# Kernel optimization log

Measured on AMD Instinct MI355X. Metric: run time of the kernel, lower is better.

Reference implementation:

```python
import jax, jax.numpy as jnp
import numpy as np
import math

E = 1024      # embed_dim
H = 16        # num_heads
HD = E // H   # head_dim
NBITS = 8


def fake_quant(x, n_bits=NBITS):
    """Symmetric per-tensor fake quantize with STE (clamp/round/dequant)."""
    qmax = 2.0 ** (n_bits - 1) - 1.0
    qmin = -(2.0 ** (n_bits - 1))
    scale = jnp.maximum(jnp.max(jnp.abs(x)) / qmax, 1e-8)
    xq = jnp.round(jnp.clip(x / scale, qmin, qmax)) * scale
    return x + jax.lax.stop_gradient(xq - x)


def setup_inputs() -> dict:
    key = jax.random.key(0)
    ks = jax.random.split(key, 7)
    L, B = 2048, 2
    query = jax.random.normal(ks[0], (L, B, E), dtype=jnp.float32)
    k_in = jax.random.normal(ks[1], (L, B, E), dtype=jnp.float32)
    v_in = jax.random.normal(ks[2], (L, B, E), dtype=jnp.float32)
    in_w = jax.random.normal(ks[3], (3 * E, E), dtype=jnp.float32) * (1.0 / math.sqrt(E))
    in_b = jax.random.normal(ks[4], (3 * E,), dtype=jnp.float32) * 0.01
    out_w = jax.random.normal(ks[5], (E, E), dtype=jnp.float32) * (1.0 / math.sqrt(E))
    out_b = jax.random.normal(ks[6], (E,), dtype=jnp.float32) * 0.01
    return {"query": query, "key": k_in, "value": v_in,
            "in_w": in_w, "in_b": in_b, "out_w": out_w, "out_b": out_b}


def reference(query, key, value, in_w, in_b, out_w, out_b):
    # NOTE: the original module ignores `key`/`value` (pure self-attention on query),
    # and its attn / softmax fake-quant lines are dead statements (results discarded).
    L, B, _ = query.shape
    Wi = fake_quant(in_w)
    Wo = fake_quant(out_w)
    # input projection: [L,B,3E]
    X = jnp.einsum('lbe,fe->lbf', query, Wi) + in_b
    X = fake_quant(X)
    Q, K, V = jnp.split(X, 3, axis=-1)  # each [L,B,E]
    # [L, B*H, HD] -> [B*H, L, HD]
    q = Q.reshape(L, B * H, HD).transpose(1, 0, 2)
    k = K.reshape(L, B * H, HD).transpose(1, 0, 2)
    v = V.reshape(L, B * H, HD).transpose(1, 0, 2)
    q = q / math.sqrt(HD)
    q = fake_quant(q)
    attn = jnp.einsum('bqd,bkd->bqk', q, k)          # [B*H, L, L]
    attn = jax.nn.softmax(attn, axis=-1)
    heads = jnp.einsum('bqk,bkd->bqd', attn, v)      # [B*H, L, HD]
    heads = fake_quant(heads)
    # [B*H, L, HD] -> [L, B*H, HD] -> [L*B, E]
    heads_r = heads.transpose(1, 0, 2).reshape(L * B, E)
    y = heads_r @ Wo.T + out_b
    y = y.reshape(L, B, E)
    return fake_quant(y)
```

## Files before the change

kernel.cpp:

```cpp
#include <hip/hip_runtime.h>
#include <math.h>

#define L_SEQ 2048
#define BATCH 2
#define EMB 1024
#define NH 16
#define HDIM 64
#define F3 3072
#define NROWS 4096

typedef __bf16 bf16_t;
typedef short s16x8 __attribute__((ext_vector_type(8)));
typedef float f32x4 __attribute__((ext_vector_type(4)));

#define MFMA16(a, b, c) __builtin_amdgcn_mfma_f32_16x16x32_bf16(a, b, c, 0, 0, 0)


__device__ __forceinline__ float u2f(unsigned u) { return __uint_as_float(u); }

__device__ __forceinline__ unsigned short bfb(bf16_t x) {
  union { bf16_t b; unsigned short u; } c; c.b = x; return c.u;
}

__device__ __forceinline__ void gload16(const bf16_t* g, bf16_t* lds) {
  __builtin_amdgcn_global_load_lds((const __attribute__((address_space(1))) void*)g,
                                   (__attribute__((address_space(3))) void*)lds, 16, 0, 0);
}

__device__ __forceinline__ void blockmax_commit(float m, unsigned* slot) {
  #pragma unroll
  for (int o = 1; o < 64; o <<= 1) m = fmaxf(m, __shfl_xor(m, o));
  __shared__ float sm_[4];
  if ((threadIdx.x & 63) == 0) sm_[threadIdx.x >> 6] = m;
  __syncthreads();
  if (threadIdx.x == 0) {
    float mm = fmaxf(fmaxf(sm_[0], sm_[1]), fmaxf(sm_[2], sm_[3]));
    atomicMax(slot, __float_as_uint(mm));
  }
}

__global__ __launch_bounds__(256) void absmax_k(const float* __restrict__ x, int n4,
                                                unsigned* __restrict__ slot) {
  const float4* x4 = (const float4*)x;
  float m = 0.0f;
  for (int i = blockIdx.x * blockDim.x + threadIdx.x; i < n4; i += gridDim.x * blockDim.x) {
    float4 v = x4[i];
    m = fmaxf(m, fmaxf(fmaxf(fabsf(v.x), fabsf(v.y)), fmaxf(fabsf(v.z), fabsf(v.w))));
  }
  blockmax_commit(m, slot);
}

__global__ __launch_bounds__(256) void quantf_k(const float* __restrict__ x,
                                                bf16_t* __restrict__ y, int n4,
                                                const unsigned* __restrict__ slots, int sloti) {
  float s = fmaxf(u2f(slots[sloti]) / 127.0f, 1e-8f);
  const float4* x4 = (const float4*)x;
  for (int i = blockIdx.x * blockDim.x + threadIdx.x; i < n4; i += gridDim.x * blockDim.x) {
    float4 v = x4[i];
    bf16_t o[4];
    o[0] = (bf16_t)rintf(fminf(fmaxf(v.x / s, -128.0f), 127.0f));
    o[1] = (bf16_t)rintf(fminf(fmaxf(v.y / s, -128.0f), 127.0f));
    o[2] = (bf16_t)rintf(fminf(fmaxf(v.z / s, -128.0f), 127.0f));
    o[3] = (bf16_t)rintf(fminf(fmaxf(v.w / s, -128.0f), 127.0f));
    *(uint2*)&y[(size_t)i * 4] = *(uint2*)o;
  }
}

__global__ __launch_bounds__(256) void quantX_k(const float* __restrict__ x,
                                                bf16_t* __restrict__ y,
                                                unsigned* __restrict__ slots) {
  float s = fmaxf(u2f(slots[2]) / 127.0f, 1e-8f);
  float qm = 0.0f;
  const int n8 = NROWS * F3 / 8;
  for (int i = blockIdx.x * blockDim.x + threadIdx.x; i < n8; i += gridDim.x * blockDim.x) {
    float4 v0 = *(const float4*)&x[(size_t)i * 8];
    float4 v1 = *(const float4*)&x[(size_t)i * 8 + 4];
    float vv[8] = {v0.x, v0.y, v0.z, v0.w, v1.x, v1.y, v1.z, v1.w};
    bf16_t o[8];
    float lm = 0.0f;
    #pragma unroll
    for (int j = 0; j < 8; ++j) {
      float q = rintf(fminf(fmaxf(vv[j] / s, -128.0f), 127.0f));
      o[j] = (bf16_t)q;
      lm = fmaxf(lm, fabsf(q));
    }
    if ((i % 384) < 128) qm = fmaxf(qm, lm);
    *(uint4*)&y[(size_t)i * 8] = *(uint4*)o;
  }
  blockmax_commit(qm, slots + 3);
}

__global__ __launch_bounds__(256) void quant_k(float* __restrict__ x, int n4,
                                               const unsigned* __restrict__ slots, int sloti) {
  float s = fmaxf(u2f(slots[sloti]) / 127.0f, 1e-8f);
  float4* x4 = (float4*)x;
  for (int i = blockIdx.x * blockDim.x + threadIdx.x; i < n4; i += gridDim.x * blockDim.x) {
    float4 v = x4[i];
    v.x = rintf(fminf(fmaxf(v.x / s, -128.0f), 127.0f)) * s;
    v.y = rintf(fminf(fmaxf(v.y / s, -128.0f), 127.0f)) * s;
    v.z = rintf(fminf(fmaxf(v.z / s, -128.0f), 127.0f)) * s;
    v.w = rintf(fminf(fmaxf(v.w / s, -128.0f), 127.0f)) * s;
    x4[i] = v;
  }
}

__global__ __launch_bounds__(256) void split_k(const float* __restrict__ x,
                                               bf16_t* __restrict__ hi,
                                               bf16_t* __restrict__ lo, int n4) {
  const float4* x4 = (const float4*)x;
  for (int i = blockIdx.x * blockDim.x + threadIdx.x; i < n4; i += gridDim.x * blockDim.x) {
    float4 v = x4[i];
    bf16_t h[4], l[4];
    float vv[4] = {v.x, v.y, v.z, v.w};
    #pragma unroll
    for (int j = 0; j < 4; ++j) {
      h[j] = (bf16_t)vv[j];
      l[j] = (bf16_t)(vv[j] - (float)h[j]);
    }
    *(uint2*)&hi[(size_t)i * 4] = *(uint2*)h;
    *(uint2*)&lo[(size_t)i * 4] = *(uint2*)l;
  }
}

__global__ __launch_bounds__(256) void vtrans_k(const bf16_t* __restrict__ X,
                                                bf16_t* __restrict__ Vt) {
  __shared__ __align__(16) bf16_t tile[64][72];
  int tt = blockIdx.x, bh = blockIdx.y;
  int b = bh >> 4, h = bh & 15;
  int t = threadIdx.x;
  #pragma unroll
  for (int i = 0; i < 2; ++i) {
    int s = t + i * 256;
    int tok = s >> 3, seg = s & 7;
    uint4 v = *(const uint4*)&X[((size_t)(tt * 64 + tok) * BATCH + b) * F3 + 2 * EMB + h * HDIM + seg * 8];
    int segs = seg ^ (tok >> 3);
    *(uint4*)&tile[tok][segs * 8] = v;
  }
  __syncthreads();
  #pragma unroll
  for (int i = 0; i < 2; ++i) {
    int s = t + i * 256;
    int d = s >> 3, tseg = s & 7;
    bf16_t o[8];
    #pragma unroll
    for (int e = 0; e < 8; ++e) {
      int tok = tseg * 8 + e;
      o[e] = tile[tok][(((d >> 3) ^ (tok >> 3)) << 3) | (d & 7)];
    }
    *(uint4*)&Vt[((size_t)bh * HDIM + d) * L_SEQ + tt * 64 + tseg * 8] = *(uint4*)o;
  }
}

template <int NPARTS>
__global__ __launch_bounds__(256) void gemm_bt_mfma_k(const bf16_t* __restrict__ A0,
                                                      const bf16_t* __restrict__ A1,
                                                      const bf16_t* __restrict__ Bm,
                                                      const float* __restrict__ bias,
                                                      float* __restrict__ C,
                                                      int M, int N, int K,
                                                      unsigned* __restrict__ slots,
                                                      int sa, int sb, int smax) {
  __shared__ __align__(16) bf16_t sbuf[2][NPARTS + 1][128][32];
  int t = threadIdx.x;
  int w = t >> 6, l = t & 63, c15 = l & 15, g = l >> 4;
  int wr = w >> 1, wc = w & 1;
  int bm = blockIdx.y * 128, bn = blockIdx.x * 128;
  f32x4 acc[4][4] = {};

  auto stage = [&](int bf, int k0) {
    #pragma unroll
    for (int i = 0; i < 2; ++i) {
      int c = i * 256 + t;
      int row = c >> 2, sg = c & 3;
      int wb = (i * 256 + w * 64) * 8;
      gload16(&A0[(size_t)(bm + row) * K + k0 + sg * 8], &sbuf[bf][0][0][0] + wb);
      if (NPARTS == 2)
        gload16(&A1[(size_t)(bm + row) * K + k0 + sg * 8], &sbuf[bf][1][0][0] + wb);
      gload16(&Bm[(size_t)(bn + row) * K + k0 + sg * 8], &sbuf[bf][NPARTS][0][0] + wb);
    }
  };

  stage(0, 0);
  __syncthreads();
  const int nk = K / 32;
  for (int kt = 0; kt < nk; ++kt) {
    int cur = kt & 1;
    if (kt + 1 < nk) stage(cur ^ 1, (kt + 1) * 32);
    s16x8 af[NPARTS][4], bf_[4];
    #pragma unroll
    for (int rt = 0; rt < 4; ++rt) {
      af[0][rt] = *(const s16x8*)&sbuf[cur][0][wr * 64 + rt * 16 + c15][g * 8];
      if (NPARTS == 2) af[1][rt] = *(const s16x8*)&sbuf[cur][1][wr * 64 + rt * 16 + c15][g * 8];
    }
    #pragma unroll
    for (int ct = 0; ct < 4; ++ct)
      bf_[ct] = *(const s16x8*)&sbuf[cur][NPARTS][wc * 64 + ct * 16 + c15][g * 8];
    __builtin_amdgcn_s_setprio(1);
    #pragma unroll
    for (int rt = 0; rt < 4; ++rt)
      #pragma unroll
      for (int ct = 0; ct < 4; ++ct) {
        acc[rt][ct] = MFMA16(af[0][rt], bf_[ct], acc[rt][ct]);
        if (NPARTS == 2) acc[rt][ct] = MFMA16(af[1][rt], bf_[ct], acc[rt][ct]);
      }
    __builtin_amdgcn_s_setprio(0);
    __syncthreads();
  }

  float s = 1.0f;
  if (sa >= 0) s *= fmaxf(u2f(slots[sa]) / 127.0f, 1e-8f);
  if (sb >= 0) s *= fmaxf(u2f(slots[sb]) / 127.0f, 1e-8f);
  float vmax = 0.0f;
  #pragma unroll
  for (int rt = 0; rt < 4; ++rt)
    #pragma unroll
    for (int r = 0; r < 4; ++r) {
      int row = bm + wr * 64 + rt * 16 + 4 * g + r;
      #pragma unroll
      for (int ct = 0; ct < 4; ++ct) {
        int col = bn + wc * 64 + ct * 16 + c15;
        float o = acc[rt][ct][r] * s + bias[col];
        vmax = fmaxf(vmax, fabsf(o));
        C[(size_t)row * N + col] = o;
      }
    }
  if (smax >= 0) blockmax_commit(vmax, slots + smax);
}

__global__ __launch_bounds__(256) void attn_mfma_k(const bf16_t* __restrict__ X,
                                                   const bf16_t* __restrict__ Vt,
                                                   float* __restrict__ heads,
                                                   unsigned* __restrict__ slots) {
  int qb = blockIdx.x, bh = blockIdx.y;
  int b = bh >> 4, h = bh & 15;
  int t = threadIdx.x;
  int w = t >> 6, l = t & 63, c15 = l & 15, g = l >> 4;

  float s_x = fmaxf(u2f(slots[2]) / 127.0f, 1e-8f);
  float s_q = fmaxf((u2f(slots[3]) * s_x) * 0.125f / 127.0f, 1e-8f);
  const float LOG2E = 1.4426950408889634f;
  float qsl2 = s_q * s_x * LOG2E;

  __shared__ __align__(16) union SmKV {
    struct { bf16_t Ks[64][72]; bf16_t Vs[64][72]; } kv;
    float Ot[4][16][69];
  } sm;
  __shared__ __align__(16) bf16_t Pl[4][16][136];

  int qrow = qb * 64 + w * 16 + c15;
  const bf16_t* qbase = X + ((size_t)qrow * BATCH + b) * F3 + h * HDIM;
  s16x8 qf0, qf1;
  {
    bf16_t qt[8];
    #pragma unroll
    for (int half = 0; half < 2; ++half) {
      *(uint4*)qt = *(const uint4*)(qbase + half * 32 + g * 8);
      #pragma unroll
      for (int j = 0; j < 8; ++j) {
        float q = ((float)qt[j] * s_x) * 0.125f;
        qt[j] = (bf16_t)rintf(fminf(fmaxf(q / s_q, -128.0f), 127.0f));
      }
      if (half == 0) qf0 = *(s16x8*)qt; else qf1 = *(s16x8*)qt;
    }
  }

  int r0 = t >> 3, sg0 = t & 7;
  const size_t tokstride = (size_t)BATCH * F3;
  const bf16_t* kp = X + (size_t)r0 * tokstride + (size_t)b * F3 + EMB + h * HDIM + sg0 * 8;
  const bf16_t* vbase = Vt + (size_t)bh * HDIM * L_SEQ;
  const bf16_t* vp = vbase + (size_t)r0 * L_SEQ + sg0 * 8;

  uint4 gk0, gk1, gv0, gv1;
  auto loadg = [&](int kt) {
    size_t ko = (size_t)kt * 64 * tokstride;
    gk0 = *(const uint4*)(kp + ko);
    gk1 = *(const uint4*)(kp + ko + 32 * tokstride);
    int vo = kt * 64;
    gv0 = *(const uint4*)(vp + vo);
    gv1 = *(const uint4*)(vp + vo + 32 * L_SEQ);
  };
  auto write_lds = [&]() {
    *(uint4*)&sm.kv.Ks[r0][sg0 * 8] = gk0;
    *(uint4*)&sm.kv.Ks[r0 + 32][sg0 * 8] = gk1;
    *(uint4*)&sm.kv.Vs[r0][sg0 * 8] = gv0;
    *(uint4*)&sm.kv.Vs[r0 + 32][sg0 * 8] = gv1;
  };

  f32x4 acc_o[4] = {};
  float m_prev = -INFINITY, lsum = 0.0f;

  loadg(0);
  write_lds();
  __syncthreads();

  const int NT = L_SEQ / 64;
  for (int kt = 0; kt < NT; ++kt) {
    f32x4 accs[4] = {};
    __builtin_amdgcn_s_setprio(1);
    #pragma unroll
    for (int ct = 0; ct < 4; ++ct) {
      s16x8 kf0 = *(const s16x8*)&sm.kv.Ks[ct * 16 + c15][g * 8];
      s16x8 kf1 = *(const s16x8*)&sm.kv.Ks[ct * 16 + c15][32 + g * 8];
      accs[ct] = MFMA16(kf0, qf0, accs[ct]);
      accs[ct] = MFMA16(kf1, qf1, accs[ct]);
    }
    __builtin_amdgcn_s_setprio(0);

    if (kt + 1 < NT) loadg(kt + 1);

    float pm = accs[0][0];
    #pragma unroll
    for (int ct = 0; ct < 4; ++ct)
      #pragma unroll
      for (int r = 0; r < 4; ++r) pm = fmaxf(pm, accs[ct][r]);
    pm = fmaxf(pm, __shfl_xor(pm, 16));
    pm = fmaxf(pm, __shfl_xor(pm, 32));
    float mnew = fmaxf(m_prev, pm);
    float f_ = __builtin_amdgcn_exp2f((m_prev - mnew) * qsl2);
    float mq = mnew * qsl2;
    float ps = 0.0f;
    #pragma unroll
    for (int ct = 0; ct < 4; ++ct) {
      float p[4];
      #pragma unroll
      for (int r = 0; r < 4; ++r) p[r] = __builtin_amdgcn_exp2f(fmaf(accs[ct][r], qsl2, -mq));
      ps += (p[0] + p[1]) + (p[2] + p[3]);
      bf16_t h_[4], l_[4];
      #pragma unroll
      for (int r = 0; r < 4; ++r) { h_[r] = (bf16_t)p[r]; l_[r] = (bf16_t)(p[r] - (float)h_[r]); }
      uint2 hiw, low;
      hiw.x = (unsigned)bfb(h_[0]) | ((unsigned)bfb(h_[1]) << 16);
      hiw.y = (unsigned)bfb(h_[2]) | ((unsigned)bfb(h_[3]) << 16);
      low.x = (unsigned)bfb(l_[0]) | ((unsigned)bfb(l_[1]) << 16);
      low.y = (unsigned)bfb(l_[2]) | ((unsigned)bfb(l_[3]) << 16);
      *(uint2*)&Pl[w][c15][ct * 16 + g * 4] = hiw;
      *(uint2*)&Pl[w][c15][64 + ct * 16 + g * 4] = low;
    }
    lsum = lsum * f_ + ps;
    m_prev = mnew;

    if (!__all(f_ == 1.0f)) {
      #pragma unroll
      for (int dt = 0; dt < 4; ++dt)
        #pragma unroll
        for (int r = 0; r < 4; ++r) acc_o[dt][r] *= f_;
    }

    s16x8 pf_h0 = *(const s16x8*)&Pl[w][c15][g * 8];
    s16x8 pf_h1 = *(const s16x8*)&Pl[w][c15][32 + g * 8];
    s16x8 pf_l0 = *(const s16x8*)&Pl[w][c15][64 + g * 8];
    s16x8 pf_l1 = *(const s16x8*)&Pl[w][c15][96 + g * 8];
    __builtin_amdgcn_s_setprio(1);
    #pragma unroll
    for (int dt = 0; dt < 4; ++dt) {
      s16x8 vf0 = *(const s16x8*)&sm.kv.Vs[dt * 16 + c15][g * 8];
      s16x8 vf1 = *(const s16x8*)&sm.kv.Vs[dt * 16 + c15][32 + g * 8];
      acc_o[dt] = MFMA16(vf0, pf_h0, acc_o[dt]);
      acc_o[dt] = MFMA16(vf1, pf_h1, acc_o[dt]);
      acc_o[dt] = MFMA16(vf0, pf_l0, acc_o[dt]);
      acc_o[dt] = MFMA16(vf1, pf_l1, acc_o[dt]);
    }
    __builtin_amdgcn_s_setprio(0);

    __syncthreads();
    if (kt + 1 < NT) write_lds();
    __syncthreads();
  }

  lsum += __shfl_xor(lsum, 16);
  lsum += __shfl_xor(lsum, 32);
  float inv = s_x / lsum;

  float hm = 0.0f;
  #pragma unroll
  for (int dt = 0; dt < 4; ++dt)
    #pragma unroll
    for (int r = 0; r < 4; ++r) {
      float o = acc_o[dt][r] * inv;
      hm = fmaxf(hm, fabsf(o));
      sm.Ot[w][c15][dt * 16 + 4 * g + r] = o;
    }
  int ql = l >> 2, cs = l & 3;
  #pragma unroll
  for (int j = 0; j < 4; ++j) {
    int cch = cs + 4 * j;
    float4 v = *(const float4*)&sm.Ot[w][ql][cch * 4];
    int row = qb * 64 + w * 16 + ql;
    *(float4*)&heads[((size_t)row * BATCH + b) * EMB + h * HDIM + cch * 4] = v;
  }
  blockmax_commit(hm, slots + 4);
}

extern "C" void kernel_launch(void* const* d_in, const int* in_sizes, int n_in,
                              void* d_out, int out_size, void* d_ws, size_t ws_size,
                              hipStream_t stream) {
  (void)in_sizes; (void)n_in; (void)out_size; (void)ws_size;
  const float* query = (const float*)d_in[0];
  const float* in_w  = (const float*)d_in[3];
  const float* in_b  = (const float*)d_in[4];
  const float* out_w = (const float*)d_in[5];
  const float* out_b = (const float*)d_in[6];
  float* out = (float*)d_out;

  unsigned* slots = (unsigned*)d_ws;
  char* p = (char*)d_ws + 256;
  bf16_t* q_hi   = (bf16_t*)p;                  p += (size_t)NROWS * EMB * 2;
  bf16_t* q_lo   = (bf16_t*)p;                  p += (size_t)NROWS * EMB * 2;
  bf16_t* Wi_int = (bf16_t*)p;                  p += (size_t)F3 * EMB * 2;
  bf16_t* Wo_int = (bf16_t*)p;                  p += (size_t)EMB * EMB * 2;
  float*  X_f32  = (float*)p;                   p += (size_t)NROWS * F3 * 4;
  bf16_t* X_int  = (bf16_t*)p;
  bf16_t* Vt     = q_hi;
  bf16_t* heads_int = (bf16_t*)X_f32;
  float*  heads_f32 = out;

  hipMemsetAsync(d_ws, 0, 256, stream);

  dim3 b256(256);
  absmax_k<<<1024, b256, 0, stream>>>(in_w, F3 * EMB / 4, slots + 0);
  absmax_k<<<512,  b256, 0, stream>>>(out_w, EMB * EMB / 4, slots + 1);
  quantf_k<<<1024, b256, 0, stream>>>(in_w, Wi_int, F3 * EMB / 4, slots, 0);
  quantf_k<<<512,  b256, 0, stream>>>(out_w, Wo_int, EMB * EMB / 4, slots, 1);

  split_k<<<2048, b256, 0, stream>>>(query, q_hi, q_lo, NROWS * EMB / 4);

  gemm_bt_mfma_k<2><<<dim3(F3 / 128, NROWS / 128), b256, 0, stream>>>(
      q_hi, q_lo, Wi_int, in_b, X_f32, NROWS, F3, EMB, slots, -1, 0, 2);

  quantX_k<<<2048, b256, 0, stream>>>(X_f32, X_int, slots);

  vtrans_k<<<dim3(L_SEQ / 64, BATCH * NH), b256, 0, stream>>>(X_int, Vt);

  attn_mfma_k<<<dim3(L_SEQ / 64, BATCH * NH), b256, 0, stream>>>(X_int, Vt, heads_f32, slots);

  quantf_k<<<1024, b256, 0, stream>>>(heads_f32, heads_int, NROWS * EMB / 4, slots, 4);

  gemm_bt_mfma_k<1><<<dim3(EMB / 128, NROWS / 128), b256, 0, stream>>>(
      heads_int, nullptr, Wo_int, out_b, out, NROWS, EMB, EMB, slots, 4, 1, 5);

  quant_k<<<1024, b256, 0, stream>>>(out, NROWS * EMB / 4, slots, 5);
}
```

Baseline: 259.3 us.

## Fuse weight prep kernels, swizzle GEMM blocks, prefetch earlier in attention

Merges the two weight absmax kernels into one and the weight quantization plus query hi/lo split into a single prep kernel, cutting launch count. The GEMM maps block ids through a grouped swizzle to improve L2 reuse of operand tiles. The attention loop issues the next tile's global loads before the QK MFMAs to overlap memory with compute. The V transpose now reads fp32 X and quantizes on the fly, adding extra read traffic.

```diff
diff --git a/kernel.cpp b/kernel.cpp
--- a/kernel.cpp
+++ b/kernel.cpp
@@ -39,15 +39,104 @@
   }
 }
 
-__global__ __launch_bounds__(256) void absmax_k(const float* __restrict__ x, int n4,
-                                                unsigned* __restrict__ slot) {
-  const float4* x4 = (const float4*)x;
-  float m = 0.0f;
+__global__ __launch_bounds__(256) void wabsmax_k(const float* __restrict__ wi,
+                                                 const float* __restrict__ wo,
+                                                 unsigned* __restrict__ slots) {
+  float m0 = 0.0f, m1 = 0.0f;
+  const int n0 = F3 * EMB / 4, n1 = EMB * EMB / 4;
+  for (int i = blockIdx.x * blockDim.x + threadIdx.x; i < n0; i += gridDim.x * blockDim.x) {
+    float4 v = ((const float4*)wi)[i];
+    m0 = fmaxf(m0, fmaxf(fmaxf(fabsf(v.x), fabsf(v.y)), fmaxf(fabsf(v.z), fabsf(v.w))));
+  }
+  for (int i = blockIdx.x * blockDim.x + threadIdx.x; i < n1; i += gridDim.x * blockDim.x) {
+    float4 v = ((const float4*)wo)[i];
+    m1 = fmaxf(m1, fmaxf(fmaxf(fabsf(v.x), fabsf(v.y)), fmaxf(fabsf(v.z), fabsf(v.w))));
+  }
+  blockmax_commit(m0, slots + 0);
+  blockmax_commit(m1, slots + 1);
+}
+
+__global__ __launch_bounds__(256) void prep_k(const float* __restrict__ wi,
+                                              const float* __restrict__ wo,
+                                              const float* __restrict__ query,
+                                              bf16_t* __restrict__ Wi_int,
+                                              bf16_t* __restrict__ Wo_int,
+                                              bf16_t* __restrict__ q_hi,
+                                              bf16_t* __restrict__ q_lo,
+                                              const unsigned* __restrict__ slots) {
+  float s0 = fmaxf(u2f(slots[0]) / 127.0f, 1e-8f);
+  float s1 = fmaxf(u2f(slots[1]) / 127.0f, 1e-8f);
+  const int n0 = F3 * EMB / 4, n1 = EMB * EMB / 4, n2 = NROWS * EMB / 4;
+  for (int i = blockIdx.x * blockDim.x + threadIdx.x; i < n0; i += gridDim.x * blockDim.x) {
+    float4 v = ((const float4*)wi)[i];
+    bf16_t o[4];
+    o[0] = (bf16_t)rintf(fminf(fmaxf(v.x / s0, -128.0f), 127.0f));
+    o[1] = (bf16_t)rintf(fminf(fmaxf(v.y / s0, -128.0f), 127.0f));
+    o[2] = (bf16_t)rintf(fminf(fmaxf(v.z / s0, -128.0f), 127.0f));
+    o[3] = (bf16_t)rintf(fminf(fmaxf(v.w / s0, -128.0f), 127.0f));
+    *(uint2*)&Wi_int[(size_t)i * 4] = *(uint2*)o;
+  }
+  for (int i = blockIdx.x * blockDim.x + threadIdx.x; i < n1; i += gridDim.x * blockDim.x) {
+    float4 v = ((const float4*)wo)[i];
+    bf16_t o[4];
+    o[0] = (bf16_t)rintf(fminf(fmaxf(v.x / s1, -128.0f), 127.0f));
+    o[1] = (bf16_t)rintf(fminf(fmaxf(v.y / s1, -128.0f), 127.0f));
+    o[2] = (bf16_t)rintf(fminf(fmaxf(v.z / s1, -128.0f), 127.0f));
+    o[3] = (bf16_t)rintf(fminf(fmaxf(v.w / s1, -128.0f), 127.0f));
+    *(uint2*)&Wo_int[(size_t)i * 4] = *(uint2*)o;
+  }
+  for (int i = blockIdx.x * blockDim.x + threadIdx.x; i < n2; i += gridDim.x * blockDim.x) {
+    float4 v = ((const float4*)query)[i];
+    bf16_t h[4], l[4];
+    float vv[4] = {v.x, v.y, v.z, v.w};
+    #pragma unroll
+    for (int j = 0; j < 4; ++j) {
+      h[j] = (bf16_t)vv[j];
+      l[j] = (bf16_t)(vv[j] - (float)h[j]);
+    }
+    *(uint2*)&q_hi[(size_t)i * 4] = *(uint2*)h;
+    *(uint2*)&q_lo[(size_t)i * 4] = *(uint2*)l;
+  }
+}
+
+__global__ __launch_bounds__(256) void quantX_k(const float* __restrict__ x,
+                                                bf16_t* __restrict__ y,
+                                                unsigned* __restrict__ slots) {
+  float s = fmaxf(u2f(slots[2]) / 127.0f, 1e-8f);
+  float qm = 0.0f;
+  const int n8 = NROWS * 256;
+  for (int i = blockIdx.x * blockDim.x + threadIdx.x; i < n8; i += gridDim.x * blockDim.x) {
+    int row = i >> 8, ch = i & 255;
+    const float* px = x + (size_t)row * F3 + ch * 8;
+    float4 v0 = *(const float4*)px;
+    float4 v1 = *(const float4*)(px + 4);
+    float vv[8] = {v0.x, v0.y, v0.z, v0.w, v1.x, v1.y, v1.z, v1.w};
+    bf16_t o[8];
+    float lm = 0.0f;
+    #pragma unroll
+    for (int j = 0; j < 8; ++j) {
+      float q = rintf(fminf(fmaxf(vv[j] / s, -128.0f), 127.0f));
+      o[j] = (bf16_t)q;
+      lm = fmaxf(lm, fabsf(q));
+    }
+    if (ch < 128) qm = fmaxf(qm, lm);
+    *(uint4*)&y[(size_t)row * F3 + ch * 8] = *(uint4*)o;
+  }
+  blockmax_commit(qm, slots + 3);
+}
+
+__global__ __launch_bounds__(256) void quant_k(float* __restrict__ x, int n4,
+                                               const unsigned* __restrict__ slots, int sloti) {
+  float s = fmaxf(u2f(slots[sloti]) / 127.0f, 1e-8f);
+  float4* x4 = (float4*)x;
   for (int i = blockIdx.x * blockDim.x + threadIdx.x; i < n4; i += gridDim.x * blockDim.x) {
     float4 v = x4[i];
-    m = fmaxf(m, fmaxf(fmaxf(fabsf(v.x), fabsf(v.y)), fmaxf(fabsf(v.z), fabsf(v.w))));
-  }
-  blockmax_commit(m, slot);
+    v.x = rintf(fminf(fmaxf(v.x / s, -128.0f), 127.0f)) * s;
+    v.y = rintf(fminf(fmaxf(v.y / s, -128.0f), 127.0f)) * s;
+    v.z = rintf(fminf(fmaxf(v.z / s, -128.0f), 127.0f)) * s;
+    v.w = rintf(fminf(fmaxf(v.w / s, -128.0f), 127.0f)) * s;
+    x4[i] = v;
+  }
 }
 
 __global__ __launch_bounds__(256) void quantf_k(const float* __restrict__ x,
@@ -66,81 +155,34 @@
   }
 }
 
-__global__ __launch_bounds__(256) void quantX_k(const float* __restrict__ x,
-                                                bf16_t* __restrict__ y,
-                                                unsigned* __restrict__ slots) {
+__global__ __launch_bounds__(256) void vtrans_k(const float* __restrict__ X,
+                                                bf16_t* __restrict__ Vt,
+                                                const unsigned* __restrict__ slots) {
   float s = fmaxf(u2f(slots[2]) / 127.0f, 1e-8f);
-  float qm = 0.0f;
-  const int n8 = NROWS * F3 / 8;
-  for (int i = blockIdx.x * blockDim.x + threadIdx.x; i < n8; i += gridDim.x * blockDim.x) {
-    float4 v0 = *(const float4*)&x[(size_t)i * 8];
-    float4 v1 = *(const float4*)&x[(size_t)i * 8 + 4];
-    float vv[8] = {v0.x, v0.y, v0.z, v0.w, v1.x, v1.y, v1.z, v1.w};
-    bf16_t o[8];
-    float lm = 0.0f;
-    #pragma unroll
-    for (int j = 0; j < 8; ++j) {
-      float q = rintf(fminf(fmaxf(vv[j] / s, -128.0f), 127.0f));
-      o[j] = (bf16_t)q;
-      lm = fmaxf(lm, fabsf(q));
-    }
-    if ((i % 384) < 128) qm = fmaxf(qm, lm);
-    *(uint4*)&y[(size_t)i * 8] = *(uint4*)o;
-  }
-  blockmax_commit(qm, slots + 3);
-}
-
-__global__ __launch_bounds__(256) void quant_k(float* __restrict__ x, int n4,
-                                               const unsigned* __restrict__ slots, int sloti) {
-  float s = fmaxf(u2f(slots[sloti]) / 127.0f, 1e-8f);
-  float4* x4 = (float4*)x;
-  for (int i = blockIdx.x * blockDim.x + threadIdx.x; i < n4; i += gridDim.x * blockDim.x) {
-    float4 v = x4[i];
-    v.x = rintf(fminf(fmaxf(v.x / s, -128.0f), 127.0f)) * s;
-    v.y = rintf(fminf(fmaxf(v.y / s, -128.0f), 127.0f)) * s;
-    v.z = rintf(fminf(fmaxf(v.z / s, -128.0f), 127.0f)) * s;
-    v.w = rintf(fminf(fmaxf(v.w / s, -128.0f), 127.0f)) * s;
-    x4[i] = v;
-  }
-}
-
-__global__ __launch_bounds__(256) void split_k(const float* __restrict__ x,
-                                               bf16_t* __restrict__ hi,
-                                               bf16_t* __restrict__ lo, int n4) {
-  const float4* x4 = (const float4*)x;
-  for (int i = blockIdx.x * blockDim.x + threadIdx.x; i < n4; i += gridDim.x * blockDim.x) {
-    float4 v = x4[i];
-    bf16_t h[4], l[4];
-    float vv[4] = {v.x, v.y, v.z, v.w};
-    #pragma unroll
-    for (int j = 0; j < 4; ++j) {
-      h[j] = (bf16_t)vv[j];
-      l[j] = (bf16_t)(vv[j] - (float)h[j]);
-    }
-    *(uint2*)&hi[(size_t)i * 4] = *(uint2*)h;
-    *(uint2*)&lo[(size_t)i * 4] = *(uint2*)l;
-  }
-}
-
-__global__ __launch_bounds__(256) void vtrans_k(const bf16_t* __restrict__ X,
-                                                bf16_t* __restrict__ Vt) {
   __shared__ __align__(16) bf16_t tile[64][72];
   int tt = blockIdx.x, bh = blockIdx.y;
   int b = bh >> 4, h = bh & 15;
   int t = threadIdx.x;
   #pragma unroll
   for (int i = 0; i < 2; ++i) {
-    int s = t + i * 256;
-    int tok = s >> 3, seg = s & 7;
-    uint4 v = *(const uint4*)&X[((size_t)(tt * 64 + tok) * BATCH + b) * F3 + 2 * EMB + h * HDIM + seg * 8];
+    int s_ = t + i * 256;
+    int tok = s_ >> 3, seg = s_ & 7;
+    const float* px = X + ((size_t)(tt * 64 + tok) * BATCH + b) * F3 + 2 * EMB + h * HDIM + seg * 8;
+    float4 v0 = *(const float4*)px;
+    float4 v1 = *(const float4*)(px + 4);
+    float vv[8] = {v0.x, v0.y, v0.z, v0.w, v1.x, v1.y, v1.z, v1.w};
+    bf16_t o[8];
+    #pragma unroll
+    for (int j = 0; j < 8; ++j)
+      o[j] = (bf16_t)rintf(fminf(fmaxf(vv[j] / s, -128.0f), 127.0f));
     int segs = seg ^ (tok >> 3);
-    *(uint4*)&tile[tok][segs * 8] = v;
+    *(uint4*)&tile[tok][segs * 8] = *(uint4*)o;
   }
   __syncthreads();
   #pragma unroll
   for (int i = 0; i < 2; ++i) {
-    int s = t + i * 256;
-    int d = s >> 3, tseg = s & 7;
+    int s_ = t + i * 256;
+    int d = s_ >> 3, tseg = s_ & 7;
     bf16_t o[8];
     #pragma unroll
     for (int e = 0; e < 8; ++e) {
@@ -164,7 +206,11 @@
   int t = threadIdx.x;
   int w = t >> 6, l = t & 63, c15 = l & 15, g = l >> 4;
   int wr = w >> 1, wc = w & 1;
-  int bm = blockIdx.y * 128, bn = blockIdx.x * 128;
+  int nx = gridDim.x;
+  int fid = blockIdx.y * nx + blockIdx.x;
+  int qq = (nx * gridDim.y) >> 3;
+  int swz = (fid & 7) * qq + (fid >> 3);
+  int bm = (swz / nx) * 128, bn = (swz % nx) * 128;
   f32x4 acc[4][4] = {};
 
   auto stage = [&](int bf, int k0) {
@@ -295,6 +341,8 @@
 
   const int NT = L_SEQ / 64;
   for (int kt = 0; kt < NT; ++kt) {
+    if (kt + 1 < NT) loadg(kt + 1);
+
     f32x4 accs[4] = {};
     __builtin_amdgcn_s_setprio(1);
     #pragma unroll
@@ -305,8 +353,6 @@
       accs[ct] = MFMA16(kf1, qf1, accs[ct]);
     }
     __builtin_amdgcn_s_setprio(0);
-
-    if (kt + 1 < NT) loadg(kt + 1);
 
     float pm = accs[0][0];
     #pragma unroll
@@ -328,13 +374,13 @@
       bf16_t h_[4], l_[4];
       #pragma unroll
       for (int r = 0; r < 4; ++r) { h_[r] = (bf16_t)p[r]; l_[r] = (bf16_t)(p[r] - (float)h_[r]); }
-      uint2 hiw, low;
-      hiw.x = (unsigned)bfb(h_[0]) | ((unsigned)bfb(h_[1]) << 16);
-      hiw.y = (unsigned)bfb(h_[2]) | ((unsigned)bfb(h_[3]) << 16);
-      low.x = (unsigned)bfb(l_[0]) | ((unsigned)bfb(l_[1]) << 16);
-      low.y = (unsigned)bfb(l_[2]) | ((unsigned)bfb(l_[3]) << 16);
-      *(uint2*)&Pl[w][c15][ct * 16 + g * 4] = hiw;
-      *(uint2*)&Pl[w][c15][64 + ct * 16 + g * 4] = low;
+      uint2 hw, lw;
+      hw.x = (unsigned)bfb(h_[0]) | ((unsigned)bfb(h_[1]) << 16);
+      hw.y = (unsigned)bfb(h_[2]) | ((unsigned)bfb(h_[3]) << 16);
+      lw.x = (unsigned)bfb(l_[0]) | ((unsigned)bfb(l_[1]) << 16);
+      lw.y = (unsigned)bfb(l_[2]) | ((unsigned)bfb(l_[3]) << 16);
+      *(uint2*)&Pl[w][c15][ct * 16 + g * 4] = hw;
+      *(uint2*)&Pl[w][c15][64 + ct * 16 + g * 4] = lw;
     }
     lsum = lsum * f_ + ps;
     m_prev = mnew;
@@ -417,19 +463,15 @@
   hipMemsetAsync(d_ws, 0, 256, stream);
 
   dim3 b256(256);
-  absmax_k<<<1024, b256, 0, stream>>>(in_w, F3 * EMB / 4, slots + 0);
-  absmax_k<<<512,  b256, 0, stream>>>(out_w, EMB * EMB / 4, slots + 1);
-  quantf_k<<<1024, b256, 0, stream>>>(in_w, Wi_int, F3 * EMB / 4, slots, 0);
-  quantf_k<<<512,  b256, 0, stream>>>(out_w, Wo_int, EMB * EMB / 4, slots, 1);
-
-  split_k<<<2048, b256, 0, stream>>>(query, q_hi, q_lo, NROWS * EMB / 4);
+  wabsmax_k<<<768, b256, 0, stream>>>(in_w, out_w, slots);
+  prep_k<<<1024, b256, 0, stream>>>(in_w, out_w, query, Wi_int, Wo_int, q_hi, q_lo, slots);
 
   gemm_bt_mfma_k<2><<<dim3(F3 / 128, NROWS / 128), b256, 0, stream>>>(
       q_hi, q_lo, Wi_int, in_b, X_f32, NROWS, F3, EMB, slots, -1, 0, 2);
 
   quantX_k<<<2048, b256, 0, stream>>>(X_f32, X_int, slots);
 
-  vtrans_k<<<dim3(L_SEQ / 64, BATCH * NH), b256, 0, stream>>>(X_int, Vt);
+  vtrans_k<<<dim3(L_SEQ / 64, BATCH * NH), b256, 0, stream>>>(X_f32, Vt, slots);
 
   attn_mfma_k<<<dim3(L_SEQ / 64, BATCH * NH), b256, 0, stream>>>(X_int, Vt, heads_f32, slots);
 
```

Result: no change. 257.3 us (-0.8%).
